# Kernel tuning notes

Hardware: AMD Instinct MI355X
Metric: run time of the kernel (lower is better)

The kernel has to match this reference:

```python
import jax, jax.numpy as jnp
import numpy as np

K_MASK = -2.3819763e+38
NUM_HEADS = 16
NUM_KV_HEADS = 8
FEATURES = 2048
HEAD_DIM = 128
WINDOW = 1024
SOFT_CAP = 50.0
B, T = 2, 2048


def apply_rope(inputs, positions, head_dim, max_wavelength=10000):
    # inputs: [B, T, N, H], positions: [B, T]
    fraction = 2 * jnp.arange(0, head_dim // 2) / head_dim
    timescale = max_wavelength ** fraction
    sinusoid_inp = positions[..., None] / timescale[None, None, :]  # [B,T,H/2]
    sinusoid_inp = sinusoid_inp[..., None, :]  # [B,T,1,H/2]
    sin = jnp.sin(sinusoid_inp)
    cos = jnp.cos(sinusoid_inp)
    first_half, second_half = jnp.split(inputs, 2, axis=-1)
    first_part = first_half * cos - second_half * sin
    second_part = second_half * cos + first_half * sin
    return jnp.concatenate([first_part, second_part], axis=-1).astype(inputs.dtype)


def setup_inputs() -> dict:
    key = jax.random.key(0)
    k1, k2, k3, k4 = jax.random.split(key, 4)
    std = 0.02
    x = jax.random.normal(k1, (B, T, FEATURES), dtype=jnp.float32)
    segment_pos = jnp.broadcast_to(jnp.arange(T, dtype=jnp.int32), (B, T))
    # causal prefill mask [B, T, T]
    attn_mask = jnp.broadcast_to(jnp.tril(jnp.ones((T, T), dtype=bool)), (B, T, T))
    wq = jax.random.normal(k2, (NUM_HEADS, FEATURES, HEAD_DIM), dtype=jnp.float32) * std
    wkv = jax.random.normal(k3, (2, NUM_KV_HEADS, FEATURES, HEAD_DIM), dtype=jnp.float32) * std
    wo = jax.random.normal(k4, (NUM_HEADS, HEAD_DIM, FEATURES), dtype=jnp.float32) * std
    return {"x": x, "segment_pos": segment_pos, "attn_mask": attn_mask,
            "wq": wq, "wkv": wkv, "wo": wo}


def reference(x, segment_pos, attn_mask, wq, wkv, wo):
    # Projections (GQA path: num_kv_heads != num_heads)
    q = jnp.einsum('BTD,NDH->BTNH', x, wq)              # [B,T,N,H]
    k = jnp.einsum('BSD,KDH->BSKH', x, wkv[0])          # [B,S,K,H]
    v = jnp.einsum('BSD,KDH->BSKH', x, wkv[1])          # [B,S,K,H]

    q = apply_rope(q, segment_pos, HEAD_DIM)
    q = q * HEAD_DIM ** (-0.5)
    k = apply_rope(k, segment_pos, HEAD_DIM)

    b, t, n, h = q.shape
    g = n // NUM_KV_HEADS
    qg = q.reshape(b, t, NUM_KV_HEADS, g, h)
    logits = jnp.einsum('BTKGH,BSKH->BTKGS', qg, k)
    s = logits.shape[-1]
    logits = logits.reshape(b, t, n, s)

    # soft cap
    logits = jnp.tanh(logits / SOFT_CAP) * SOFT_CAP

    # sliding-window mask combined with attn_mask
    cache_positions = jnp.arange(s)[None, None, :]
    sp = segment_pos[:, :, None]
    sliding_mask = (cache_positions >= sp - WINDOW + 1) & (cache_positions <= sp + WINDOW - 1)
    mask = sliding_mask & attn_mask  # [B,T,S]

    padded_logits = jnp.where(mask[:, :, None, :], logits, K_MASK)
    probs = jax.nn.softmax(padded_logits, axis=-1).astype(k.dtype)

    pg = probs.reshape(b, t, NUM_KV_HEADS, g, s)
    encoded = jnp.einsum('BTKGS,BSKH->BTKGH', pg, v).reshape(b, t, n, h)
    attn_output = jnp.einsum('BTNH,NHD->BTD', encoded, wo)
    return attn_output
```

## Files before the change

kernel.cpp:

```cpp
#include <hip/hip_runtime.h>

typedef unsigned short u16;
typedef unsigned int u32;
typedef __attribute__((ext_vector_type(8))) short bfx8;
typedef __attribute__((ext_vector_type(4))) float fx4;

static __device__ __forceinline__ float b2f(u16 u) {
    union { float f; u32 i; } c; c.i = ((u32)u) << 16; return c.f;
}
static __device__ __forceinline__ u16 f2b(float f) {
    union { float f; u32 i; } c; c.f = f;
    u32 r = c.i + 0x7FFFu + ((c.i >> 16) & 1u);
    return (u16)(r >> 16);
}
typedef const __attribute__((address_space(1))) unsigned int* gas1;
typedef __attribute__((address_space(3))) unsigned int* las3;
static __device__ __forceinline__ void gll16(const void* g, void* l) {
    __builtin_amdgcn_global_load_lds((gas1)g, (las3)l, 16, 0, 0);
}

__global__ __launch_bounds__(256) void k_convert_x(const float* __restrict__ x, u16* __restrict__ xb) {
    size_t i = ((size_t)blockIdx.x * 256 + threadIdx.x) * 8;
    float4 a = *(const float4*)(x + i);
    float4 b = *(const float4*)(x + i + 4);
    union { u16 e[8]; uint4 v; } o;
    o.e[0] = f2b(a.x); o.e[1] = f2b(a.y); o.e[2] = f2b(a.z); o.e[3] = f2b(a.w);
    o.e[4] = f2b(b.x); o.e[5] = f2b(b.y); o.e[6] = f2b(b.z); o.e[7] = f2b(b.w);
    *(uint4*)(xb + i) = o.v;
}

__global__ __launch_bounds__(256) void k_pack_w1(const float* __restrict__ wq, const float* __restrict__ wkv,
                                                 u16* __restrict__ wb1) {
    __shared__ float t[128 * 33];
    int ci = blockIdx.x;
    int k0 = blockIdx.y << 5;
    int c0 = ci << 7;
    const float* src;
    if (ci < 16)      src = wq  + (size_t)ci * 2048 * 128;
    else if (ci < 24) src = wkv + (size_t)(ci - 16) * 2048 * 128;
    else              src = wkv + (size_t)(8 + ci - 24) * 2048 * 128;
    int tid = threadIdx.x;
#pragma unroll
    for (int i = 0; i < 16; i++) {
        int idx = i * 256 + tid;
        int kk = idx >> 7, cc = idx & 127;
        t[cc * 33 + kk] = src[(size_t)(k0 + kk) * 128 + cc];
    }
    __syncthreads();
#pragma unroll
    for (int i = 0; i < 16; i++) {
        int idx = i * 256 + tid;
        int cc = idx >> 5, kk = idx & 31;
        wb1[(size_t)(c0 + cc) * 2048 + k0 + kk] = f2b(t[cc * 33 + kk]);
    }
}

__global__ __launch_bounds__(256) void k_pack_w2(const float* __restrict__ wo, u16* __restrict__ wb2) {
    __shared__ float t[128 * 33];
    int c0 = blockIdx.x << 7;
    int k0 = blockIdx.y << 5;
    int tid = threadIdx.x;
#pragma unroll
    for (int i = 0; i < 16; i++) {
        int idx = i * 256 + tid;
        int kk = idx >> 7, cc = idx & 127;
        t[cc * 33 + kk] = wo[(size_t)(k0 + kk) * 2048 + c0 + cc];
    }
    __syncthreads();
#pragma unroll
    for (int i = 0; i < 16; i++) {
        int idx = i * 256 + tid;
        int cc = idx >> 5, kk = idx & 31;
        wb2[(size_t)(c0 + cc) * 2048 + k0 + kk] = f2b(t[cc * 33 + kk]);
    }
}

template <int BM, int OUT_BF16>
__global__ __launch_bounds__(512, 2) void k_gemm256(const u16* __restrict__ A, const u16* __restrict__ Bt,
                                                    void* __restrict__ C, int M, int N, int K) {
    constexpr int MF = BM / 32;
    constexpr int NA = BM / 16;
    constexpr int FR = NA + 16;
    constexpr int LPW = FR / 8;
    __shared__ u16 lds[4 * FR * 512];

    int tid = threadIdx.x, wave = tid >> 6, lane = tid & 63;
    int quad = lane >> 4, l16 = lane & 15;
    int wm = wave >> 2, wn = wave & 3;

    int nwg = gridDim.x * gridDim.y;
    int bid = blockIdx.y * gridDim.x + blockIdx.x;
    int swz = (bid & 7) * (nwg >> 3) + (bid >> 3);
    int bx = swz % gridDim.x, by = swz / gridDim.x;
    int r0 = by * BM, c0 = bx << 8;

    fx4 zero = {0.f, 0.f, 0.f, 0.f};
    fx4 acc[MF][4];
#pragma unroll
    for (int m = 0; m < MF; m++)
#pragma unroll
        for (int n = 0; n < 4; n++) acc[m][n] = zero;

    const u16* gsrc[LPW];
#pragma unroll
    for (int j = 0; j < LPW; j++) {
        int fw = wave * LPW + j;
        gsrc[j] = (fw < NA ? A + (size_t)(r0 + fw * 16 + l16) * K
                           : Bt + (size_t)(c0 + (fw - NA) * 16 + l16) * K) + quad * 8;
    }
    u16* ldst = lds + wave * (LPW * 512);

    int NT = K >> 5;
#pragma unroll
    for (int p = 0; p < 3; p++)
#pragma unroll
        for (int j = 0; j < LPW; j++) gll16(gsrc[j] + p * 32, ldst + p * (FR * 512) + j * 512);

    for (int t = 0; t < NT; ++t) {
        int rem = NT - 1 - t;
        if (rem >= 2)      asm volatile("s_waitcnt vmcnt(%0)" : : "n"(2 * LPW) : "memory");
        else if (rem == 1) asm volatile("s_waitcnt vmcnt(%0)" : : "n"(LPW) : "memory");
        else               asm volatile("s_waitcnt vmcnt(0)" : : : "memory");
        __builtin_amdgcn_s_barrier();

        const u16* Fb = lds + (t & 3) * (FR * 512);
        const u16* Ab = Fb + wm * (MF * 512);
        const u16* Bb = Fb + (NA + wn * 4) * 512;
        bfx8 bf[4], af[4];
#pragma unroll
        for (int n = 0; n < 4; n++) bf[n] = *(const bfx8*)(Bb + n * 512 + lane * 8);
#pragma unroll
        for (int m = 0; m < 4; m++) af[m] = *(const bfx8*)(Ab + m * 512 + lane * 8);
        if (t + 3 < NT) {
            u16* dst = lds + ((t + 3) & 3) * (FR * 512) + wave * (LPW * 512);
#pragma unroll
            for (int j = 0; j < LPW; j++) gll16(gsrc[j] + (size_t)(t + 3) * 32, dst + j * 512);
        }
        __builtin_amdgcn_s_barrier();
        __builtin_amdgcn_s_setprio(1);
#pragma unroll
        for (int m = 0; m < 4; m++)
#pragma unroll
            for (int n = 0; n < 4; n++)
                acc[m][n] = __builtin_amdgcn_mfma_f32_16x16x32_bf16(af[m], bf[n], acc[m][n], 0, 0, 0);
        __builtin_amdgcn_s_setprio(0);
        if constexpr (MF == 8) {
            __builtin_amdgcn_s_barrier();
#pragma unroll
            for (int m = 0; m < 4; m++) af[m] = *(const bfx8*)(Ab + (4 + m) * 512 + lane * 8);
            __builtin_amdgcn_s_barrier();
            __builtin_amdgcn_s_setprio(1);
#pragma unroll
            for (int m = 0; m < 4; m++)
#pragma unroll
                for (int n = 0; n < 4; n++)
                    acc[4 + m][n] = __builtin_amdgcn_mfma_f32_16x16x32_bf16(af[m], bf[n], acc[4 + m][n], 0, 0, 0);
            __builtin_amdgcn_s_setprio(0);
        }
    }
#pragma unroll
    for (int m = 0; m < MF; m++)
#pragma unroll
        for (int n = 0; n < 4; n++) {
            int col = c0 + wn * 64 + n * 16 + l16;
#pragma unroll
            for (int r = 0; r < 4; r++) {
                int row = r0 + wm * (BM / 2) + m * 16 + quad * 4 + r;
                float v = acc[m][n][r];
                if (OUT_BF16) ((u16*)C)[(size_t)row * N + col] = f2b(v);
                else          ((float*)C)[(size_t)row * N + col] = v;
            }
        }
}

__global__ __launch_bounds__(256) void k_rope(const u16* __restrict__ qkv, u16* __restrict__ Qb,
                                              u16* __restrict__ Kb, u16* __restrict__ Vb) {
    __shared__ float sc[128];
    int bt = blockIdx.x;
    int b = bt >> 11, t = bt & 2047;
    const u16* row = qkv + (size_t)bt * 4096;
    int tid = threadIdx.x;
    float tf = (float)t;
    const float RS = 0.08838834764831845f;
    const float LT = 0.20762050593046f;
    if (tid < 64) {
        float ang = tf * exp2f(-LT * (float)tid);
        float s, c; sincosf(ang, &s, &c);
        sc[tid] = s; sc[tid + 64] = c;
    }
    __syncthreads();
#pragma unroll
    for (int i = 0; i < 4; i++) {
        int idx = tid + i * 256;
        int n = idx >> 6, hp = idx & 63;
        float x1 = b2f(row[n * 128 + hp]);
        float x2 = b2f(row[n * 128 + hp + 64]);
        float s = sc[hp], c = sc[hp + 64];
        size_t o = ((size_t)(b * 16 + n) * 2048 + t) * 128 + hp;
        Qb[o]      = f2b((x1 * c - x2 * s) * RS);
        Qb[o + 64] = f2b((x2 * c + x1 * s) * RS);
    }
#pragma unroll
    for (int i = 0; i < 2; i++) {
        int idx = tid + i * 256;
        int kh = idx >> 6, hp = idx & 63;
        float x1 = b2f(row[2048 + kh * 128 + hp]);
        float x2 = b2f(row[2048 + kh * 128 + hp + 64]);
        float s = sc[hp], c = sc[hp + 64];
        size_t o = ((size_t)(b * 8 + kh) * 2048 + t) * 128 + hp;
        Kb[o]      = f2b(x1 * c - x2 * s);
        Kb[o + 64] = f2b(x2 * c + x1 * s);
    }
#pragma unroll
    for (int i = 0; i < 4; i++) {
        int idx = tid + i * 256;
        int kh = idx >> 7, h = idx & 127;
        Vb[((size_t)(b * 8 + kh) * 2048 + t) * 128 + h] = row[3072 + idx];
    }
}

__global__ __launch_bounds__(256) void k_transpose_v(const u16* __restrict__ Vb, u16* __restrict__ Vt) {
    __shared__ u16 t[128 * 136];
    int bk = blockIdx.y;
    int t0 = blockIdx.x << 7;
    const u16* src = Vb + ((size_t)bk * 2048 + t0) * 128;
    u16* dst = Vt + (size_t)bk * 128 * 2048 + t0;
    int tid = threadIdx.x;
#pragma unroll
    for (int it = 0; it < 8; it++) {
        int ch = tid + it * 256;
        int tt = ch >> 4, c8 = (ch & 15) << 3;
        *(uint4*)(t + tt * 136 + c8) = *(const uint4*)(src + (size_t)tt * 128 + c8);
    }
    __syncthreads();
#pragma unroll
    for (int it = 0; it < 8; it++) {
        int ch = tid + it * 256;
        int h = ch >> 4, s8 = (ch & 15) << 3;
        union { uint4 v; u16 e[8]; } vv;
#pragma unroll
        for (int j = 0; j < 8; j++) vv.e[j] = t[(s8 + j) * 136 + h];
        *(uint4*)(dst + (size_t)h * 2048 + s8) = vv.v;
    }
}

__global__ __launch_bounds__(256, 4) void k_attn(const u16* __restrict__ Qb, const u16* __restrict__ Kb,
                                                 const u16* __restrict__ Vt, u16* __restrict__ enc) {
    __shared__ u16 Ks[16 * 512];
    __shared__ u16 Vs[16 * 512];
    __shared__ u16 Pl[4 * 1024];
    int t0 = blockIdx.x << 6;
    int n = blockIdx.y, b = blockIdx.z, kh = n >> 1;
    int tid = threadIdx.x, wave = tid >> 6, lane = tid & 63;
    int quad = lane >> 4, l16 = lane & 15;
    int tw = t0 + (wave << 4);
    const u16* Qp = Qb + (size_t)(b * 16 + n) * 2048 * 128;
    const u16* Kp = Kb + (size_t)(b * 8 + kh) * 2048 * 128;
    const u16* Vp = Vt + (size_t)(b * 8 + kh) * 128 * 2048;

    bfx8 aq[4];
#pragma unroll
    for (int kb = 0; kb < 4; kb++)
        aq[kb] = *(const bfx8*)(Qp + (size_t)(tw + l16) * 128 + kb * 32 + quad * 8);

    const u16* kgp[4]; const u16* vgp[4];
    u16 *kls[4], *vls[4];
#pragma unroll
    for (int q = 0; q < 4; q++) {
        int f = wave * 4 + q;
        kgp[q] = Kp + (size_t)((f >> 2) * 16 + l16) * 128 + (f & 3) * 32 + quad * 8;
        kls[q] = Ks + f * 512;
        vgp[q] = Vp + (size_t)((f >> 1) * 16 + l16) * 2048 + (f & 1) * 32 + quad * 8;
        vls[q] = Vs + f * 512;
    }
    u16* Pw = Pl + wave * 1024;

    fx4 zero = {0.f, 0.f, 0.f, 0.f};
    fx4 o_acc[8];
#pragma unroll
    for (int hb = 0; hb < 8; hb++) o_acc[hb] = zero;
    float lsum[4] = {0.f, 0.f, 0.f, 0.f};

    const float C1 = 0.057707801635559f;
    const float C2 = 144.269504088896f;

    int s_lo = t0 - 1023; if (s_lo < 0) s_lo = 0;
    int ts1 = t0 >> 6;
    for (int ts = (s_lo >> 6); ts <= ts1; ts++) {
        int s0 = ts << 6;
        __syncthreads();
#pragma unroll
        for (int q = 0; q < 4; q++) {
            gll16(kgp[q] + (size_t)s0 * 128, kls[q]);
            gll16(vgp[q] + s0, vls[q]);
        }
        __syncthreads();

        if (s0 <= tw + 15 && s0 + 63 >= tw - 1023) {
#pragma unroll
            for (int nb = 0; nb < 4; nb++) {
                int sb = s0 + (nb << 4);
                int base0 = ((nb >> 1) * 64 + ((nb & 1) * 2 + (l16 >> 3)) * 16 + quad * 4) * 8 + (l16 & 7);
                if (sb <= tw + 15 && sb + 15 >= tw - 1023) {
                    fx4 sacc = zero;
#pragma unroll
                    for (int kb = 0; kb < 4; kb++) {
                        bfx8 bk = *(const bfx8*)(Ks + (nb * 4 + kb) * 512 + lane * 8);
                        sacc = __builtin_amdgcn_mfma_f32_16x16x32_bf16(aq[kb], bk, sacc, 0, 0, 0);
                    }
                    int sg = sb + l16;
#pragma unroll
                    for (int r = 0; r < 4; r++) {
                        int tg = tw + quad * 4 + r;
                        float u = __builtin_amdgcn_exp2f(sacc[r] * C1);
                        float p = __builtin_amdgcn_exp2f(-C2 * __builtin_amdgcn_rcpf(u + 1.f));
                        p = (sg <= tg && sg >= tg - 1023) ? p : 0.f;
                        lsum[r] += p;
                        Pw[base0 + r * 8] = f2b(p);
                    }
                } else {
#pragma unroll
                    for (int r = 0; r < 4; r++) Pw[base0 + r * 8] = 0;
                }
            }
            __builtin_amdgcn_s_waitcnt(0);
            bfx8 pf[2];
#pragma unroll
            for (int kk = 0; kk < 2; kk++)
                pf[kk] = *(const bfx8*)(Pw + kk * 512 + lane * 8);
#pragma unroll
            for (int hb = 0; hb < 8; hb++)
#pragma unroll
                for (int kk = 0; kk < 2; kk++) {
                    bfx8 vf = *(const bfx8*)(Vs + (hb * 2 + kk) * 512 + lane * 8);
                    o_acc[hb] = __builtin_amdgcn_mfma_f32_16x16x32_bf16(pf[kk], vf, o_acc[hb], 0, 0, 0);
                }
        }
    }
#pragma unroll
    for (int r = 0; r < 4; r++) {
#pragma unroll
        for (int off = 1; off < 16; off <<= 1)
            lsum[r] += __shfl_xor(lsum[r], off);
        lsum[r] = 1.0f / lsum[r];
    }
#pragma unroll
    for (int hb = 0; hb < 8; hb++) {
        int h = hb * 16 + l16;
#pragma unroll
        for (int r = 0; r < 4; r++) {
            int tg = tw + quad * 4 + r;
            enc[((size_t)(b * 2048 + tg) * 16 + n) * 128 + h] = f2b(o_acc[hb][r] * lsum[r]);
        }
    }
}

extern "C" void kernel_launch(void* const* d_in, const int* in_sizes, int n_in,
                              void* d_out, int out_size, void* d_ws, size_t ws_size,
                              hipStream_t stream) {
    const float* x   = (const float*)d_in[0];
    const float* wq  = (const float*)d_in[3];
    const float* wkv = (const float*)d_in[4];
    const float* wo  = (const float*)d_in[5];
    char* ws = (char*)d_ws;
    const size_t MiB = 1024 * 1024;
    u16* xb  = (u16*)(ws);
    u16* wb1 = (u16*)(ws + 16 * MiB);
    u16* qkv = (u16*)(ws + 32 * MiB);
    u16* Qb  = (u16*)(ws);
    u16* Kb  = (u16*)(ws + 16 * MiB);
    u16* Vb  = (u16*)(ws + 24 * MiB);
    u16* enc = (u16*)(ws + 32 * MiB);
    u16* wb2 = (u16*)(ws + 48 * MiB);
    u16* Vt  = (u16*)(ws + 56 * MiB);

    k_convert_x<<<4096, 256, 0, stream>>>(x, xb);
    k_pack_w1<<<dim3(32, 64), 256, 0, stream>>>(wq, wkv, wb1);
    k_gemm256<256, 1><<<dim3(16, 16), 512, 0, stream>>>(xb, wb1, qkv, 4096, 4096, 2048);
    k_rope<<<4096, 256, 0, stream>>>(qkv, Qb, Kb, Vb);
    k_transpose_v<<<dim3(16, 16), 256, 0, stream>>>(Vb, Vt);
    k_pack_w2<<<dim3(16, 64), 256, 0, stream>>>(wo, wb2);
    k_attn<<<dim3(32, 16, 2), 256, 0, stream>>>(Qb, Kb, Vt, enc);
    k_gemm256<128, 0><<<dim3(8, 32), 512, 0, stream>>>(enc, wb2, d_out, 4096, 2048, 2048);
}
```

Before: 377.3 us.

## Double-buffer K/V tiles in attention kernel and add unmasked fast path

Splits the K and V shared-memory tiles into two buffers and prefetches the next 64-key tile with global_load_lds while the current tile is computed. Raw barriers plus explicit vmcnt waits replace the paired __syncthreads, so tile loading overlaps the softmax and MFMA work. Tiles lying fully inside the causal/sliding window take a separate path that skips the per-element mask check. LDS use doubles and launch bounds drop from 4 to 2 blocks per SM, which can reduce occupancy and latency hiding.

```diff
diff --git a/kernel.cpp b/kernel.cpp
--- a/kernel.cpp
+++ b/kernel.cpp
@@ -244,10 +244,10 @@
     }
 }
 
-__global__ __launch_bounds__(256, 4) void k_attn(const u16* __restrict__ Qb, const u16* __restrict__ Kb,
+__global__ __launch_bounds__(256, 2) void k_attn(const u16* __restrict__ Qb, const u16* __restrict__ Kb,
                                                  const u16* __restrict__ Vt, u16* __restrict__ enc) {
-    __shared__ u16 Ks[16 * 512];
-    __shared__ u16 Vs[16 * 512];
+    __shared__ u16 Ks[2][16 * 512];
+    __shared__ u16 Vs[2][16 * 512];
     __shared__ u16 Pl[4 * 1024];
     int t0 = blockIdx.x << 6;
     int n = blockIdx.y, b = blockIdx.z, kh = n >> 1;
@@ -264,14 +264,11 @@
         aq[kb] = *(const bfx8*)(Qp + (size_t)(tw + l16) * 128 + kb * 32 + quad * 8);
 
     const u16* kgp[4]; const u16* vgp[4];
-    u16 *kls[4], *vls[4];
 #pragma unroll
     for (int q = 0; q < 4; q++) {
         int f = wave * 4 + q;
         kgp[q] = Kp + (size_t)((f >> 2) * 16 + l16) * 128 + (f & 3) * 32 + quad * 8;
-        kls[q] = Ks + f * 512;
         vgp[q] = Vp + (size_t)((f >> 1) * 16 + l16) * 2048 + (f & 1) * 32 + quad * 8;
-        vls[q] = Vs + f * 512;
     }
     u16* Pw = Pl + wave * 1024;
 
@@ -285,45 +282,84 @@
     const float C2 = 144.269504088896f;
 
     int s_lo = t0 - 1023; if (s_lo < 0) s_lo = 0;
-    int ts1 = t0 >> 6;
-    for (int ts = (s_lo >> 6); ts <= ts1; ts++) {
+    int ts0 = s_lo >> 6, ts1 = t0 >> 6;
+
+#pragma unroll
+    for (int q = 0; q < 4; q++) {
+        int f = wave * 4 + q;
+        gll16(kgp[q] + (size_t)(ts0 << 6) * 128, Ks[0] + f * 512);
+        gll16(vgp[q] + (ts0 << 6), Vs[0] + f * 512);
+    }
+
+    for (int ts = ts0; ts <= ts1; ts++) {
+        int cur = (ts - ts0) & 1;
         int s0 = ts << 6;
-        __syncthreads();
-#pragma unroll
-        for (int q = 0; q < 4; q++) {
-            gll16(kgp[q] + (size_t)s0 * 128, kls[q]);
-            gll16(vgp[q] + s0, vls[q]);
-        }
-        __syncthreads();
+        __builtin_amdgcn_s_barrier();
+        if (ts < ts1) {
+            int s1 = (ts + 1) << 6;
+#pragma unroll
+            for (int q = 0; q < 4; q++) {
+                int f = wave * 4 + q;
+                gll16(kgp[q] + (size_t)s1 * 128, Ks[cur ^ 1] + f * 512);
+                gll16(vgp[q] + s1, Vs[cur ^ 1] + f * 512);
+            }
+            asm volatile("s_waitcnt vmcnt(8)" : : : "memory");
+        } else {
+            asm volatile("s_waitcnt vmcnt(0)" : : : "memory");
+        }
+        __builtin_amdgcn_s_barrier();
 
         if (s0 <= tw + 15 && s0 + 63 >= tw - 1023) {
-#pragma unroll
-            for (int nb = 0; nb < 4; nb++) {
-                int sb = s0 + (nb << 4);
-                int base0 = ((nb >> 1) * 64 + ((nb & 1) * 2 + (l16 >> 3)) * 16 + quad * 4) * 8 + (l16 & 7);
-                if (sb <= tw + 15 && sb + 15 >= tw - 1023) {
+            const u16* Kc = Ks[cur];
+            const u16* Vc = Vs[cur];
+            bool full = (s0 + 63 <= tw) && (s0 >= tw - 1008);
+            if (full) {
+#pragma unroll
+                for (int nb = 0; nb < 4; nb++) {
                     fx4 sacc = zero;
 #pragma unroll
                     for (int kb = 0; kb < 4; kb++) {
-                        bfx8 bk = *(const bfx8*)(Ks + (nb * 4 + kb) * 512 + lane * 8);
+                        bfx8 bk = *(const bfx8*)(Kc + (nb * 4 + kb) * 512 + lane * 8);
                         sacc = __builtin_amdgcn_mfma_f32_16x16x32_bf16(aq[kb], bk, sacc, 0, 0, 0);
                     }
-                    int sg = sb + l16;
+                    int base0 = ((nb >> 1) * 64 + ((nb & 1) * 2 + (l16 >> 3)) * 16 + quad * 4) * 8 + (l16 & 7);
 #pragma unroll
                     for (int r = 0; r < 4; r++) {
-                        int tg = tw + quad * 4 + r;
                         float u = __builtin_amdgcn_exp2f(sacc[r] * C1);
                         float p = __builtin_amdgcn_exp2f(-C2 * __builtin_amdgcn_rcpf(u + 1.f));
-                        p = (sg <= tg && sg >= tg - 1023) ? p : 0.f;
                         lsum[r] += p;
                         Pw[base0 + r * 8] = f2b(p);
                     }
-                } else {
-#pragma unroll
-                    for (int r = 0; r < 4; r++) Pw[base0 + r * 8] = 0;
+                }
+            } else {
+#pragma unroll
+                for (int nb = 0; nb < 4; nb++) {
+                    int sb = s0 + (nb << 4);
+                    int base0 = ((nb >> 1) * 64 + ((nb & 1) * 2 + (l16 >> 3)) * 16 + quad * 4) * 8 + (l16 & 7);
+                    if (sb <= tw + 15 && sb + 15 >= tw - 1023) {
+                        fx4 sacc = zero;
+#pragma unroll
+                        for (int kb = 0; kb < 4; kb++) {
+                            bfx8 bk = *(const bfx8*)(Kc + (nb * 4 + kb) * 512 + lane * 8);
+                            sacc = __builtin_amdgcn_mfma_f32_16x16x32_bf16(aq[kb], bk, sacc, 0, 0, 0);
+                        }
+                        int sg = sb + l16;
+#pragma unroll
+                        for (int r = 0; r < 4; r++) {
+                            int tg = tw + quad * 4 + r;
+                            float u = __builtin_amdgcn_exp2f(sacc[r] * C1);
+                            float p = __builtin_amdgcn_exp2f(-C2 * __builtin_amdgcn_rcpf(u + 1.f));
+                            p = (sg <= tg && sg >= tg - 1023) ? p : 0.f;
+                            lsum[r] += p;
+                            Pw[base0 + r * 8] = f2b(p);
+                        }
+                    } else {
+#pragma unroll
+                        for (int r = 0; r < 4; r++) Pw[base0 + r * 8] = 0;
+                    }
                 }
             }
-            __builtin_amdgcn_s_waitcnt(0);
+            asm volatile("s_waitcnt lgkmcnt(0)" : : : "memory");
             bfx8 pf[2];
 #pragma unroll
             for (int kk = 0; kk < 2; kk++)
@@ -332,7 +368,7 @@
             for (int hb = 0; hb < 8; hb++)
 #pragma unroll
                 for (int kk = 0; kk < 2; kk++) {
-                    bfx8 vf = *(const bfx8*)(Vs + (hb * 2 + kk) * 512 + lane * 8);
+                    bfx8 vf = *(const bfx8*)(Vc + (hb * 2 + kk) * 512 + lane * 8);
                     o_acc[hb] = __builtin_amdgcn_mfma_f32_16x16x32_bf16(pf[kk], vf, o_acc[hb], 0, 0, 0);
                 }
         }
```

Result: no change. 383.4 us (+1.6%).
